# Kernel tuning notes

Hardware: AMD Instinct MI355X
Metric: run time of the kernel (lower is better)

The kernel has to match this reference:

```python
import jax, jax.numpy as jnp
import numpy as np

LOC = 200 * 200 + 1   # location vocab
E = 100               # loc_emb_size
H = 100               # hidden_neurons (== input size of STLSTM)
D = 12                # temporal/spatial slot embedding dim
NSLOT = 92


def setup_inputs() -> dict:
    key = jax.random.key(0)
    ks = jax.random.split(key, 24)
    B, T = 1024, 256
    inp = {}
    inp["traj"] = jax.random.randint(ks[0], (B, T), 0, LOC)
    inp["lennew"] = jax.random.randint(ks[1], (B, T), 0, T)
    inp["traj_len"] = 255  # static scalar (loop runs traj_len+1 steps)
    inp["tu"] = jax.random.randint(ks[2], (B, T), 0, NSLOT)
    inp["tl"] = jax.random.randint(ks[3], (B, T), 0, NSLOT)
    inp["tu_slot"] = jax.random.randint(ks[4], (B, T), 0, NSLOT)
    inp["tl_slot"] = jax.random.randint(ks[5], (B, T), 0, NSLOT)
    inp["su"] = jax.random.randint(ks[6], (B, T), 0, NSLOT)
    inp["sl"] = jax.random.randint(ks[7], (B, T), 0, NSLOT)
    inp["su_slot"] = jax.random.randint(ks[8], (B, T), 0, NSLOT)
    inp["sl_slot"] = jax.random.randint(ks[9], (B, T), 0, NSLOT)
    # learned parameters
    inp["emb_loc"] = jax.random.normal(ks[10], (LOC, E), jnp.float32) * 0.02
    inp["emb_t"] = jax.random.normal(ks[11], (NSLOT, D), jnp.float32) * 0.02
    inp["emb_s"] = jax.random.normal(ks[12], (NSLOT, D), jnp.float32) * 0.02
    inp["W_ih"] = jax.random.normal(ks[13], (E, 4 * H), jnp.float32) * 0.05
    inp["W_hh"] = jax.random.normal(ks[14], (H, 4 * H), jnp.float32) * 0.05
    inp["b"] = jnp.zeros((4 * H,), jnp.float32)
    inp["W_xt"] = jax.random.normal(ks[15], (E, H), jnp.float32) * 0.05
    inp["W_tt"] = jax.random.normal(ks[16], (D, H), jnp.float32) * 0.05
    inp["b_t"] = jnp.zeros((H,), jnp.float32)
    inp["W_xs"] = jax.random.normal(ks[17], (E, H), jnp.float32) * 0.05
    inp["W_ss"] = jax.random.normal(ks[18], (D, H), jnp.float32) * 0.05
    inp["b_s"] = jnp.zeros((H,), jnp.float32)
    return inp


def reference(traj, lennew, traj_len, tu, tl, tu_slot, tl_slot, su, sl,
              su_slot, sl_slot, emb_loc, emb_t, emb_s, W_ih, W_hh, b,
              W_xt, W_tt, b_t, W_xs, W_ss, b_s):
    steps = int(traj_len) + 1  # static python int -> static slice
    x = emb_loc[traj[:, :steps]]            # [B, S, E] (dropout is identity in eval)
    dtype = x.dtype

    def interp(up_e, low_e, up_d, low_d):
        # linear interpolation between upper/lower slot embeddings
        up = up_d[:, :steps].astype(dtype)[..., None]
        low = low_d[:, :steps].astype(dtype)[..., None]
        return (up * low_e + low * up_e) / jnp.maximum(up + low, 1.0)

    Tq = interp(emb_t[tu[:, :steps]], emb_t[tl[:, :steps]], tu_slot, tl_slot)  # [B,S,D]
    Sq = interp(emb_s[su[:, :steps]], emb_s[sl[:, :steps]], su_slot, sl_slot)  # [B,S,D]

    B = traj.shape[0]
    h0 = jnp.zeros((B, H), dtype)
    c0 = jnp.zeros((B, H), dtype)
    xs = (x.swapaxes(0, 1), Tq.swapaxes(0, 1), Sq.swapaxes(0, 1))  # time-major

    def step(carry, inp):
        h, c = carry
        xt, tg, sg = inp
        gates = xt @ W_ih + h @ W_hh + b           # [B, 4H]
        i, f, g, o = jnp.split(gates, 4, axis=-1)
        i = jax.nn.sigmoid(i)
        f = jax.nn.sigmoid(f)
        g = jnp.tanh(g)
        o = jax.nn.sigmoid(o)
        tgate = jax.nn.sigmoid(xt @ W_xt + tg @ W_tt + b_t)  # temporal gate
        sgate = jax.nn.sigmoid(xt @ W_xs + sg @ W_ss + b_s)  # spatial gate
        c = f * c + i * tgate * sgate * g
        h = o * jnp.tanh(c)
        return (h, c), None

    (h, c), _ = jax.lax.scan(step, (h0, c0), xs)
    # model returns h at index traj_len, which is the final hidden state
    return h
```

## Files before the change

### kernel.cpp

```cpp
#include <hip/hip_runtime.h>

#define B_    1024
#define T_    256
#define LOCN  40001
#define E_    100
#define H_    100
#define NC    600

constexpr int PROWS = 16;
constexpr int PPAD  = 20;

__global__ __launch_bounds__(320) void proj_loc_kernel(
    const float* __restrict__ emb_loc,
    const float* __restrict__ W_ih,
    const float* __restrict__ W_xt,
    const float* __restrict__ W_xs,
    const float* __restrict__ b,
    const float* __restrict__ b_t,
    const float* __restrict__ b_s,
    float* __restrict__ P)
{
    __shared__ __attribute__((aligned(16))) float aT[E_][PPAD];
    const int tid  = threadIdx.x;
    const int row0 = blockIdx.x * PROWS;

    for (int i = tid; i < PROWS * E_; i += 320) {
        int r = i / E_, k = i - r * E_;
        int rr = row0 + r;
        float v = 0.f;
        if (rr < LOCN) v = emb_loc[rr * E_ + k];
        aT[k][r] = v;
    }
    __syncthreads();
    if (tid >= 300) return;

    for (int cc = 0; cc < 2; ++cc) {
        const int c = tid + cc * 300;
        const float* wp; int stride; float bias;
        if (c < 400)      { wp = W_ih + c;         stride = 400; bias = b[c]; }
        else if (c < 500) { wp = W_xt + (c - 400); stride = 100; bias = b_t[c - 400]; }
        else              { wp = W_xs + (c - 500); stride = 100; bias = b_s[c - 500]; }

        float acc[PROWS];
        #pragma unroll
        for (int r = 0; r < PROWS; ++r) acc[r] = bias;

        for (int k = 0; k < E_; ++k) {
            float w = wp[(size_t)k * stride];
            #pragma unroll
            for (int r = 0; r < PROWS; ++r) acc[r] += aT[k][r] * w;
        }
        #pragma unroll
        for (int r = 0; r < PROWS; ++r) {
            int rr = row0 + r;
            if (rr < LOCN) P[(size_t)rr * NC + c] = acc[r];
        }
    }
}

__global__ void proj_ts_kernel(
    const float* __restrict__ emb_t, const float* __restrict__ emb_s,
    const float* __restrict__ W_tt,  const float* __restrict__ W_ss,
    float* __restrict__ P_t, float* __restrict__ P_s)
{
    int idx = blockIdx.x * 256 + threadIdx.x;
    if (idx >= 2 * 92 * H_) return;
    int which = idx / (92 * H_);
    int rem   = idx - which * (92 * H_);
    int r = rem / H_, c = rem - r * H_;
    const float* e = which ? emb_s : emb_t;
    const float* W = which ? W_ss : W_tt;
    float acc = 0.f;
    #pragma unroll
    for (int k = 0; k < 12; ++k) acc += e[r * 12 + k] * W[k * H_ + c];
    (which ? P_s : P_t)[rem] = acc;
}

constexpr int RB = 4;
constexpr int NT = 1024;
constexpr int HP = 104;

__global__ __launch_bounds__(NT, 4) void lstm_rec_kernel(
    const int* __restrict__ traj,
    const int* __restrict__ traj_len_p,
    const int* __restrict__ tu,      const int* __restrict__ tl,
    const int* __restrict__ tu_slot, const int* __restrict__ tl_slot,
    const int* __restrict__ su,      const int* __restrict__ sl,
    const int* __restrict__ su_slot, const int* __restrict__ sl_slot,
    const float* __restrict__ P,
    const float* __restrict__ P_t,
    const float* __restrict__ P_s,
    const float* __restrict__ W_hh,
    float* __restrict__ out)
{
    __shared__ __attribute__((aligned(16))) float h_lds[RB][HP];
    __shared__ float gates_lds[RB][400];
    __shared__ float tsg_lds[RB][H_];
    __shared__ int   loc_lds[2][RB];

    const int tid = threadIdx.x;
    const int b0  = blockIdx.x * RB;
    int steps = traj_len_p[0] + 1;
    if (steps > T_) steps = T_;
    steps = __builtin_amdgcn_readfirstlane(steps);

    const bool isGate = tid < 800;
    const int  half = tid & 1;
    const int  n    = tid >> 1;
    const int  kb   = half * 52;

    for (int i = tid; i < RB * HP; i += NT) ((float*)h_lds)[i] = 0.f;
    if (tid < RB) loc_lds[0][tid] = traj[(b0 + tid) * T_];

    float w[52];
    if (isGate) {
        #pragma unroll
        for (int j = 0; j < 52; ++j) {
            const int k = kb + j;
            w[j] = (k < 100) ? W_hh[k * 400 + n] : 0.f;
        }
        #pragma unroll
        for (int j = 0; j < 52; ++j) asm volatile("" : "+v"(w[j]));
    }

    const int er = tid / 100;
    const int eh = tid - er * 100;
    float c_reg = 0.f, hval = 0.f;
    __syncthreads();

    for (int t = 0; t < steps; ++t) {
        const int buf = t & 1;

        if (tid >= 960 && tid < 964) {
            const int r = tid - 960;
            if (t + 1 < steps) loc_lds[buf ^ 1][r] = traj[(b0 + r) * T_ + t + 1];
        }

        if (isGate) {
            float gacc[RB] = {0.f, 0.f, 0.f, 0.f};
            if (half == 0) {
                #pragma unroll
                for (int r = 0; r < RB; ++r)
                    gacc[r] = P[(size_t)loc_lds[buf][r] * NC + n];
            }
            float acc[RB];
            #pragma unroll
            for (int r = 0; r < RB; ++r) acc[r] = gacc[r];
            #pragma unroll
            for (int j4 = 0; j4 < 13; ++j4) {
                #pragma unroll
                for (int r = 0; r < RB; ++r) {
                    const float4 hv = *(const float4*)(&h_lds[r][kb + j4 * 4]);
                    acc[r] += hv.x * w[j4 * 4 + 0];
                    acc[r] += hv.y * w[j4 * 4 + 1];
                    acc[r] += hv.z * w[j4 * 4 + 2];
                    acc[r] += hv.w * w[j4 * 4 + 3];
                }
            }
            const float v0 = acc[0] + __shfl_xor(acc[0], 1);
            const float v1 = acc[1] + __shfl_xor(acc[1], 1);
            const float v2 = acc[2] + __shfl_xor(acc[2], 1);
            const float v3 = acc[3] + __shfl_xor(acc[3], 1);
            const bool  isg = (n >= 200 && n < 300);
            const float va  = half ? v2 : v0;
            const float vb  = half ? v3 : v1;
            const float xa  = isg ? 2.f * va : va;
            const float xb  = isg ? 2.f * vb : vb;
            const float sa  = 1.f / (1.f + expf(-xa));
            const float sb  = 1.f / (1.f + expf(-xb));
            const float aa  = isg ? (2.f * sa - 1.f) : sa;
            const float ab  = isg ? (2.f * sb - 1.f) : sb;
            const int   rA  = half * 2;
            gates_lds[rA][n]     = aa;
            gates_lds[rA + 1][n] = ab;
        }

        if (tid >= 832 && tid < 932) {
            const int hx = tid - 832;
            #pragma unroll
            for (int r = 0; r < RB; ++r) {
                const int off = (b0 + r) * T_ + t;
                const int loc = loc_lds[buf][r];
                const float gpt = P[(size_t)loc * NC + 400 + hx];
                const float upt = (float)tu_slot[off];
                const float lot = (float)tl_slot[off];
                const int   uit = tu[off], lit = tl[off];
                const float ivt = (upt * P_t[lit * H_ + hx] + lot * P_t[uit * H_ + hx])
                                  / fmaxf(upt + lot, 1.f);
                const float tv  = 1.f / (1.f + expf(-(gpt + ivt)));
                const float gps = P[(size_t)loc * NC + 500 + hx];
                const float ups = (float)su_slot[off];
                const float los = (float)sl_slot[off];
                const int   uis = su[off], lis = sl[off];
                const float ivs = (ups * P_s[lis * H_ + hx] + los * P_s[uis * H_ + hx])
                                  / fmaxf(ups + los, 1.f);
                const float sv  = 1.f / (1.f + expf(-(gps + ivs)));
                tsg_lds[r][hx] = tv * sv;
            }
        }
        __syncthreads();

        if (tid < 400) {
            const float i_g = gates_lds[er][eh];
            const float f_g = gates_lds[er][100 + eh];
            const float g_g = gates_lds[er][200 + eh];
            const float o_g = gates_lds[er][300 + eh];
            const float tsg = tsg_lds[er][eh];
            c_reg = f_g * c_reg + i_g * tsg * g_g;
            hval  = o_g * tanhf(c_reg);
            h_lds[er][eh] = hval;
        }
        __syncthreads();
    }

    if (tid < 400) out[b0 * H_ + tid] = hval;
}

extern "C" void kernel_launch(void* const* d_in, const int* in_sizes, int n_in,
                              void* d_out, int out_size, void* d_ws, size_t ws_size,
                              hipStream_t stream) {
    const int*   traj     = (const int*)  d_in[0];
    const int*   traj_len = (const int*)  d_in[2];
    const int*   tu       = (const int*)  d_in[3];
    const int*   tl       = (const int*)  d_in[4];
    const int*   tu_slot  = (const int*)  d_in[5];
    const int*   tl_slot  = (const int*)  d_in[6];
    const int*   su       = (const int*)  d_in[7];
    const int*   sl       = (const int*)  d_in[8];
    const int*   su_slot  = (const int*)  d_in[9];
    const int*   sl_slot  = (const int*)  d_in[10];
    const float* emb_loc  = (const float*)d_in[11];
    const float* emb_t    = (const float*)d_in[12];
    const float* emb_s    = (const float*)d_in[13];
    const float* W_ih     = (const float*)d_in[14];
    const float* W_hh     = (const float*)d_in[15];
    const float* b        = (const float*)d_in[16];
    const float* W_xt     = (const float*)d_in[17];
    const float* W_tt     = (const float*)d_in[18];
    const float* b_t      = (const float*)d_in[19];
    const float* W_xs     = (const float*)d_in[20];
    const float* W_ss     = (const float*)d_in[21];
    const float* b_s      = (const float*)d_in[22];

    float* P   = (float*)d_ws;
    float* P_t = P + (size_t)LOCN * NC;
    float* P_s = P_t + 92 * H_;

    proj_loc_kernel<<<(LOCN + PROWS - 1) / PROWS, 320, 0, stream>>>(
        emb_loc, W_ih, W_xt, W_xs, b, b_t, b_s, P);
    proj_ts_kernel<<<(2 * 92 * H_ + 255) / 256, 256, 0, stream>>>(
        emb_t, emb_s, W_tt, W_ss, P_t, P_s);
    lstm_rec_kernel<<<B_ / RB, NT, 0, stream>>>(
        traj, traj_len, tu, tl, tu_slot, tl_slot, su, sl, su_slot, sl_slot,
        P, P_t, P_s, W_hh, (float*)d_out);
}
```

Baseline: 897.1 us.

## Split recurrent matvec into 4-way K chunks with two columns per thread

Each thread now covers two gate columns over a 28-wide K slice, where before it covered one column over a 52-wide half. Each LDS float4 load of h is reused for two columns, which cuts LDS traffic per FMA in the serial recurrence. The block shrinks to 960 threads and the h row padding grows to 112. In exchange the reduction needs two shuffle stages, the gather of projected inputs is spread across threads, and the helper thread indices shift.

```diff
diff --git a/kernel.cpp b/kernel.cpp
--- a/kernel.cpp
+++ b/kernel.cpp
@@ -77,8 +77,8 @@
 }
 
 constexpr int RB = 4;
-constexpr int NT = 1024;
-constexpr int HP = 104;
+constexpr int NT = 960;
+constexpr int HP = 112;
 
 __global__ __launch_bounds__(NT, 4) void lstm_rec_kernel(
     const int* __restrict__ traj,
@@ -105,22 +105,30 @@
     steps = __builtin_amdgcn_readfirstlane(steps);
 
     const bool isGate = tid < 800;
-    const int  half = tid & 1;
-    const int  n    = tid >> 1;
-    const int  kb   = half * 52;
+    const int  p   = tid >> 2;
+    const int  kq  = tid & 3;
+    const int  kb  = kq * 28;
+    const int  c0  = 2 * p;
+    const int  csel  = kq >> 1;
+    const int  rbase = (kq & 1) * 2;
+    const int  acol  = c0 + csel;
 
     for (int i = tid; i < RB * HP; i += NT) ((float*)h_lds)[i] = 0.f;
     if (tid < RB) loc_lds[0][tid] = traj[(b0 + tid) * T_];
 
-    float w[52];
+    float w0[28], w1[28];
     if (isGate) {
         #pragma unroll
-        for (int j = 0; j < 52; ++j) {
+        for (int j = 0; j < 28; ++j) {
             const int k = kb + j;
-            w[j] = (k < 100) ? W_hh[k * 400 + n] : 0.f;
-        }
-        #pragma unroll
-        for (int j = 0; j < 52; ++j) asm volatile("" : "+v"(w[j]));
+            w0[j] = (k < 100) ? W_hh[k * 400 + c0]     : 0.f;
+            w1[j] = (k < 100) ? W_hh[k * 400 + c0 + 1] : 0.f;
+        }
+        #pragma unroll
+        for (int j = 0; j < 28; ++j) {
+            asm volatile("" : "+v"(w0[j]));
+            asm volatile("" : "+v"(w1[j]));
+        }
     }
 
     const int er = tid / 100;
@@ -131,48 +139,59 @@
     for (int t = 0; t < steps; ++t) {
         const int buf = t & 1;
 
-        if (tid >= 960 && tid < 964) {
-            const int r = tid - 960;
+        if (tid >= 944 && tid < 948) {
+            const int r = tid - 944;
             if (t + 1 < steps) loc_lds[buf ^ 1][r] = traj[(b0 + r) * T_ + t + 1];
         }
 
         if (isGate) {
-            float gacc[RB] = {0.f, 0.f, 0.f, 0.f};
-            if (half == 0) {
-                #pragma unroll
-                for (int r = 0; r < RB; ++r)
-                    gacc[r] = P[(size_t)loc_lds[buf][r] * NC + n];
-            }
-            float acc[RB];
-            #pragma unroll
-            for (int r = 0; r < RB; ++r) acc[r] = gacc[r];
-            #pragma unroll
-            for (int j4 = 0; j4 < 13; ++j4) {
+            const int locA = loc_lds[buf][rbase];
+            const int locB = loc_lds[buf][rbase + 1];
+            const float gpA = P[(size_t)locA * NC + acol];
+            const float gpB = P[(size_t)locB * NC + acol];
+
+            float acc[RB][2];
+            #pragma unroll
+            for (int r = 0; r < RB; ++r) { acc[r][0] = 0.f; acc[r][1] = 0.f; }
+            #pragma unroll
+            for (int j4 = 0; j4 < 7; ++j4) {
                 #pragma unroll
                 for (int r = 0; r < RB; ++r) {
                     const float4 hv = *(const float4*)(&h_lds[r][kb + j4 * 4]);
-                    acc[r] += hv.x * w[j4 * 4 + 0];
-                    acc[r] += hv.y * w[j4 * 4 + 1];
-                    acc[r] += hv.z * w[j4 * 4 + 2];
-                    acc[r] += hv.w * w[j4 * 4 + 3];
+                    acc[r][0] += hv.x * w0[j4 * 4 + 0];
+                    acc[r][0] += hv.y * w0[j4 * 4 + 1];
+                    acc[r][0] += hv.z * w0[j4 * 4 + 2];
+                    acc[r][0] += hv.w * w0[j4 * 4 + 3];
+                    acc[r][1] += hv.x * w1[j4 * 4 + 0];
+                    acc[r][1] += hv.y * w1[j4 * 4 + 1];
+                    acc[r][1] += hv.z * w1[j4 * 4 + 2];
+                    acc[r][1] += hv.w * w1[j4 * 4 + 3];
                 }
             }
-            const float v0 = acc[0] + __shfl_xor(acc[0], 1);
-            const float v1 = acc[1] + __shfl_xor(acc[1], 1);
-            const float v2 = acc[2] + __shfl_xor(acc[2], 1);
-            const float v3 = acc[3] + __shfl_xor(acc[3], 1);
-            const bool  isg = (n >= 200 && n < 300);
-            const float va  = half ? v2 : v0;
-            const float vb  = half ? v3 : v1;
-            const float xa  = isg ? 2.f * va : va;
-            const float xb  = isg ? 2.f * vb : vb;
-            const float sa  = 1.f / (1.f + expf(-xa));
-            const float sb  = 1.f / (1.f + expf(-xb));
-            const float aa  = isg ? (2.f * sa - 1.f) : sa;
-            const float ab  = isg ? (2.f * sb - 1.f) : sb;
-            const int   rA  = half * 2;
-            gates_lds[rA][n]     = aa;
-            gates_lds[rA + 1][n] = ab;
+            float red[RB][2];
+            #pragma unroll
+            for (int r = 0; r < RB; ++r) {
+                #pragma unroll
+                for (int c = 0; c < 2; ++c) {
+                    float v = acc[r][c];
+                    v += __shfl_xor(v, 1);
+                    v += __shfl_xor(v, 2);
+                    red[r][c] = v;
+                }
+            }
+            const float sumA = rbase ? (csel ? red[2][1] : red[2][0])
+                                     : (csel ? red[0][1] : red[0][0]);
+            const float sumB = rbase ? (csel ? red[3][1] : red[3][0])
+                                     : (csel ? red[1][1] : red[1][0]);
+            const bool  isg = (acol >= 200 && acol < 300);
+            const float vA  = sumA + gpA;
+            const float vB  = sumB + gpB;
+            const float xA  = isg ? 2.f * vA : vA;
+            const float xB  = isg ? 2.f * vB : vB;
+            const float sA  = 1.f / (1.f + expf(-xA));
+            const float sB  = 1.f / (1.f + expf(-xB));
+            gates_lds[rbase][acol]     = isg ? (2.f * sA - 1.f) : sA;
+            gates_lds[rbase + 1][acol] = isg ? (2.f * sB - 1.f) : sB;
         }
 
         if (tid >= 832 && tid < 932) {
```

Result: no change. 886.4 us (-1.2%).
